# Kernel tuning notes

Hardware: AMD Instinct MI355X
Metric: run time of the kernel (lower is better)

## Reference

```python
import jax, jax.numpy as jnp
import numpy as np

D_MODEL = 2048
N_HEADS = 16
D_K = D_MODEL // N_HEADS
MAX_SEQ_LEN = 2048


def _rotary_tables(dim, max_seq_len):
    angular_freq = (1.0 / 10000.0) ** jnp.linspace(0.0, 1.0, dim // 2, dtype=jnp.float32)
    t = jnp.arange(max_seq_len, dtype=jnp.float32)
    theta = jnp.einsum('i,j->ij', t, angular_freq)  # [S, dk/2]
    return jnp.cos(theta), jnp.sin(theta)


def _apply_rotary(x, cos, sin):
    # x: [B, H, S, dk]; cos/sin: [S, dk/2]
    seq_len = x.shape[-2]
    c = cos[:seq_len][None, None]
    s = sin[:seq_len][None, None]
    x1, x2 = jnp.split(x, 2, axis=-1)
    y1 = x1 * c - x2 * s
    y2 = x1 * s + x2 * c
    return jnp.concatenate([y1, y2], axis=-1).astype(x.dtype)


def setup_inputs() -> dict:
    key = jax.random.key(0)
    k_x, k_qkv, k_o = jax.random.split(key, 3)
    B, S = 2, 2048
    x = jax.random.normal(k_x, (B, S, D_MODEL), dtype=jnp.float32)
    scale = 1.0 / np.sqrt(D_MODEL)
    w_qkv = jax.random.normal(k_qkv, (3 * D_MODEL, D_MODEL), dtype=jnp.float32) * scale
    w_o = jax.random.normal(k_o, (D_MODEL, D_MODEL), dtype=jnp.float32) * scale
    return {"x": x, "w_qkv": w_qkv, "w_o": w_o}


def reference(x, w_qkv, w_o):
    B, S, _ = x.shape
    cos, sin = _rotary_tables(D_K, MAX_SEQ_LEN)
    qkv = jnp.einsum('bsd,ed->bse', x, w_qkv)  # [B, S, 3*d_model]
    qkv = qkv.reshape(B, S, 3, N_HEADS, D_K).transpose(2, 0, 3, 1, 4)  # [3,B,H,S,dk]
    Q, K, V = qkv[0], qkv[1], qkv[2]
    Q = _apply_rotary(Q, cos, sin)
    K = _apply_rotary(K, cos, sin)
    scale = 1.0 / np.sqrt(D_K)
    scores = jnp.einsum('bhqd,bhkd->bhqk', Q, K) * scale
    causal = jnp.tril(jnp.ones((S, S), dtype=bool))
    scores = jnp.where(causal[None, None], scores, jnp.finfo(scores.dtype).min)
    attn = jax.nn.softmax(scores, axis=-1)
    out = jnp.einsum('bhqk,bhkd->bhqd', attn, V)  # [B,H,S,dk]
    out = out.transpose(0, 2, 1, 3).reshape(B, S, D_MODEL)
    return jnp.einsum('bsd,ed->bse', out, w_o)
```

## Files before the change

### kernel.cpp

```cpp
#include <hip/hip_runtime.h>
#include <hip/hip_bf16.h>


typedef __bf16 bf16;
typedef __bf16 bf16x4 __attribute__((ext_vector_type(4)));
typedef __bf16 bf16x8 __attribute__((ext_vector_type(8)));
typedef float f32x4 __attribute__((ext_vector_type(4)));
typedef float f32x16 __attribute__((ext_vector_type(16)));
typedef int i32x4 __attribute__((ext_vector_type(4)));

#define DEV __device__ __forceinline__

DEV void gll16(const void* g, void* lds_base_wave_uniform) {
  __builtin_amdgcn_global_load_lds((const __attribute__((address_space(1))) void*)g,
                                   (__attribute__((address_space(3))) void*)lds_base_wave_uniform,
                                   16, 0, 0);
}

DEV f32x4 mfma16(bf16x8 a, bf16x8 b, f32x4 c) {
  return __builtin_amdgcn_mfma_f32_16x16x32_bf16(a, b, c, 0, 0, 0);
}
DEV f32x16 mfma32(bf16x8 a, bf16x8 b, f32x16 c) {
  return __builtin_amdgcn_mfma_f32_32x32x16_bf16(a, b, c, 0, 0, 0);
}

DEV int cvtpk(float lo, float hi) {
  int r;
  asm("v_cvt_pk_bf16_f32 %0, %1, %2" : "=v"(r) : "v"(lo), "v"(hi));
  return r;
}

__global__ __launch_bounds__(256) void prep_all(const float* __restrict__ x,
                                                const float* __restrict__ wqkv,
                                                const float* __restrict__ wo,
                                                bf16* __restrict__ xb,
                                                bf16* __restrict__ wqkvb,
                                                bf16* __restrict__ wob,
                                                float* __restrict__ ctab,
                                                float* __restrict__ stab) {
  const int b = blockIdx.x;
  if (b < 12288) {
    const float* in;
    bf16* out;
    int bb = b;
    if (b < 4096) {
      in = x; out = xb;
    } else if (b < 10240) {
      in = wqkv; out = wqkvb; bb -= 4096;
    } else {
      in = wo; out = wob; bb -= 10240;
    }
    const int i = (bb * 256 + threadIdx.x) << 3;
    float4 a = *(const float4*)(in + i);
    float4 c = *(const float4*)(in + i + 4);
    bf16x8 o;
    o[0] = (bf16)a.x; o[1] = (bf16)a.y; o[2] = (bf16)a.z; o[3] = (bf16)a.w;
    o[4] = (bf16)c.x; o[5] = (bf16)c.y; o[6] = (bf16)c.z; o[7] = (bf16)c.w;
    *(bf16x8*)(out + i) = o;
  } else {
    const int id = (b - 12288) * 256 + threadIdx.x;
    const int s = id >> 6, j = id & 63;
    float freq = powf(10000.0f, -(float)j / 63.0f);
    float th = (float)s * freq;
    ctab[id] = cosf(th);
    stab[id] = sinf(th);
  }
}

__global__ __launch_bounds__(512, 2) void gemm384(const bf16* __restrict__ A,
                                                  const bf16* __restrict__ Bt,
                                                  bf16* __restrict__ q_out,
                                                  bf16* __restrict__ k_out,
                                                  bf16* __restrict__ v_out,
                                                  const float* __restrict__ ctab,
                                                  const float* __restrict__ stab) {
  constexpr int K = 2048, NKT = 64;
  constexpr int BUFB = 40960;
  __shared__ char lds[3 * BUFB];
  const int id = blockIdx.x;
  const int swz = (id & 7) * 32 + (id >> 3);
  const int bx = swz & 15, by = swz >> 4;
  const int m0 = by << 8;
  const int n0 = bx * 384;
  const int tid = threadIdx.x, w = tid >> 6, l = tid & 63;
  const int wm = w >> 2, wn = w & 3;
  const int lsl = (l & 7) ^ ((l >> 3) & 7);
  const int srow = ((l >> 3) << 1) + (lsl >> 2);
  const int scol = (lsl & 3) << 3;

  auto STAGE = [&](int t, char* base) {
    const int k0 = t << 5;
#pragma unroll
    for (int c = 0; c < 2; ++c) {
      const int row = (c << 7) + (w << 4) + srow;
      gll16(A + (size_t)(m0 + row) * K + k0 + scol, base + (c << 13) + (w << 10));
    }
#pragma unroll
    for (int c = 0; c < 3; ++c) {
      const int row = (c << 7) + (w << 4) + srow;
      gll16(Bt + (size_t)(n0 + row) * K + k0 + scol, base + 16384 + (c << 13) + (w << 10));
    }
  };

  f32x4 acc[8][6] = {};

  STAGE(0, (char*)lds);
  STAGE(1, (char*)lds + BUFB);
  asm volatile("s_waitcnt vmcnt(5)" ::: "memory");
  __builtin_amdgcn_s_barrier();

#pragma unroll 1
  for (int t = 0, bi = 0, bj = 2; t < NKT; ++t) {
    char* rbase = (char*)lds + bi * BUFB;
    bf16x8 bfr[6];
#pragma unroll
    for (int j = 0; j < 6; ++j) {
      const int row = ((j >> 1) << 7) + ((j & 1) << 6) + (wn << 4) + (l & 15);
      const int sr = row >> 1;
      bfr[j] = *(const bf16x8*)(rbase + 16384 + sr * 128 +
                                (((((row & 1) << 2) | (l >> 4)) ^ (sr & 7)) << 4));
    }
    bf16x8 af[4];
#pragma unroll
    for (int i = 0; i < 4; ++i) {
      const int row = (wm << 7) + (i << 4) + (l & 15);
      const int sr = row >> 1;
      af[i] = *(const bf16x8*)(rbase + sr * 128 +
                               (((((row & 1) << 2) | (l >> 4)) ^ (sr & 7)) << 4));
    }
    if (t + 2 < NKT) STAGE(t + 2, (char*)lds + bj * BUFB);
    asm volatile("s_waitcnt lgkmcnt(0)" ::: "memory");
    __builtin_amdgcn_sched_barrier(0);
    __builtin_amdgcn_s_setprio(1);
#pragma unroll
    for (int i = 0; i < 4; ++i)
#pragma unroll
      for (int j = 0; j < 6; ++j)
        acc[i][j] = mfma16(af[i], bfr[j], acc[i][j]);
    __builtin_amdgcn_s_setprio(0);
#pragma unroll
    for (int i = 0; i < 4; ++i) {
      const int row = (wm << 7) + 64 + (i << 4) + (l & 15);
      const int sr = row >> 1;
      af[i] = *(const bf16x8*)(rbase + sr * 128 +
                               (((((row & 1) << 2) | (l >> 4)) ^ (sr & 7)) << 4));
    }
    asm volatile("s_waitcnt lgkmcnt(0)" ::: "memory");
    __builtin_amdgcn_sched_barrier(0);
    __builtin_amdgcn_s_setprio(1);
#pragma unroll
    for (int i = 0; i < 4; ++i)
#pragma unroll
      for (int j = 0; j < 6; ++j)
        acc[4 + i][j] = mfma16(af[i], bfr[j], acc[4 + i][j]);
    __builtin_amdgcn_s_setprio(0);
    if (t + 2 < NKT) {
      asm volatile("s_waitcnt vmcnt(5)" ::: "memory");
    } else if (t + 2 == NKT) {
      asm volatile("s_waitcnt vmcnt(0)" ::: "memory");
    }
    __builtin_amdgcn_sched_barrier(0);
    __builtin_amdgcn_s_barrier();
    bi = (bi == 2) ? 0 : bi + 1;
    bj = (bj == 2) ? 0 : bj + 1;
  }

  const int d2 = (wn << 4) + (l & 15);
#pragma unroll
  for (int i = 0; i < 8; ++i) {
    const int mbase = m0 + (wm << 7) + (i << 4) + ((l >> 4) << 2);
    const int b_ = mbase >> 11, sbase = mbase & 2047;
    float cc[4], ss[4];
    if (((n0 + 256) >> 11) == 1 || (n0 >> 11) == 1) {
#pragma unroll
      for (int r = 0; r < 4; ++r) {
        cc[r] = ctab[((sbase + r) << 6) + d2];
        ss[r] = stab[((sbase + r) << 6) + d2];
      }
    }
#pragma unroll
    for (int p = 0; p < 3; ++p) {
      const int nb = n0 + (p << 7);
      const int which = nb >> 11;
      const int h = (nb >> 7) & 15;
      if (which == 0) {
        const size_t base = (((size_t)((b_ << 4) | h)) * 2048 + sbase) * 128;
#pragma unroll
        for (int r = 0; r < 4; ++r) {
          q_out[base + ((size_t)r << 7) + d2]      = (bf16)acc[i][2 * p][r];
          q_out[base + ((size_t)r << 7) + d2 + 64] = (bf16)acc[i][2 * p + 1][r];
        }
      } else if (which == 1) {
        const size_t base = (((size_t)((b_ << 4) | h)) * 2048 + sbase) * 128;
#pragma unroll
        for (int r = 0; r < 4; ++r) {
          const float x1 = acc[i][2 * p][r], x2 = acc[i][2 * p + 1][r];
          k_out[base + ((size_t)r << 7) + d2]      = (bf16)(x1 * cc[r] - x2 * ss[r]);
          k_out[base + ((size_t)r << 7) + d2 + 64] = (bf16)(x1 * ss[r] + x2 * cc[r]);
        }
      } else {
        bf16x4 v1, v2;
#pragma unroll
        for (int r = 0; r < 4; ++r) {
          v1[r] = (bf16)acc[i][2 * p][r];
          v2[r] = (bf16)acc[i][2 * p + 1][r];
        }
        const size_t hb = ((size_t)((b_ << 4) | h) << 18);
        *(bf16x4*)(v_out + hb + ((size_t)d2 << 11) + sbase) = v1;
        *(bf16x4*)(v_out + hb + ((size_t)(d2 + 64) << 11) + sbase) = v2;
      }
    }
  }
}

template <int NTN>
__global__ __launch_bounds__(256, 2) void gemm_o(const bf16* __restrict__ A,
                                                 const bf16* __restrict__ Bt,
                                                 float* __restrict__ f_out) {
  constexpr int K = 2048, NKT = 64;
  constexpr int BUFB = 16384;
  __shared__ char lds[3 * BUFB];
  const int nwg = 32 * NTN;
  const int id = blockIdx.x;
  const int swz = (id & 7) * (nwg >> 3) + (id >> 3);
  const int bx = swz % NTN, by = swz / NTN;
  const int m0 = by << 7, n0 = bx << 7;
  const int tid = threadIdx.x, w = tid >> 6, l = tid & 63;
  const int wm = w >> 1, wn = w & 1;
  const int lsl = (l & 7) ^ ((l >> 3) & 7);
  const int srow = ((l >> 3) << 1) + (lsl >> 2);
  const int scol = (lsl & 3) << 3;

  auto STAGE = [&](int t, char* base) {
    const int k0 = t << 5;
#pragma unroll
    for (int c = 0; c < 2; ++c) {
      const int row = (c << 6) + (w << 4) + srow;
      gll16(A + (size_t)(m0 + row) * K + k0 + scol, base + (c << 12) + (w << 10));
      gll16(Bt + (size_t)(n0 + row) * K + k0 + scol, base + 8192 + (c << 12) + (w << 10));
    }
  };

  f32x4 acc[4][4] = {};

  STAGE(0, (char*)lds);
  STAGE(1, (char*)lds + BUFB);
  asm volatile("s_waitcnt vmcnt(4)" ::: "memory");
  __builtin_amdgcn_s_barrier();

#pragma unroll 1
  for (int t = 0, bi = 0, bj = 2; t < NKT; ++t) {
    char* rbase = (char*)lds + bi * BUFB;
    bf16x8 af[4], bfr[4];
#pragma unroll
    for (int i = 0; i < 4; ++i) {
      const int row = (wm << 6) + (i << 4) + (l & 15);
      const int sr = row >> 1;
      af[i] = *(const bf16x8*)(rbase + sr * 128 +
                               (((((row & 1) << 2) | (l >> 4)) ^ (sr & 7)) << 4));
    }
#pragma unroll
    for (int j = 0; j < 4; ++j) {
      const int row = (wn << 6) + (j << 4) + (l & 15);
      const int sr = row >> 1;
      bfr[j] = *(const bf16x8*)(rbase + 8192 + sr * 128 +
                                (((((row & 1) << 2) | (l >> 4)) ^ (sr & 7)) << 4));
    }
    if (t + 2 < NKT) STAGE(t + 2, (char*)lds + bj * BUFB);
    asm volatile("s_waitcnt lgkmcnt(0)" ::: "memory");
    __builtin_amdgcn_sched_barrier(0);
    __builtin_amdgcn_s_setprio(1);
#pragma unroll
    for (int i = 0; i < 4; ++i)
#pragma unroll
      for (int j = 0; j < 4; ++j)
        acc[i][j] = mfma16(af[i], bfr[j], acc[i][j]);
    __builtin_amdgcn_s_setprio(0);
    if (t + 2 < NKT) {
      asm volatile("s_waitcnt vmcnt(4)" ::: "memory");
    } else if (t + 2 == NKT) {
      asm volatile("s_waitcnt vmcnt(0)" ::: "memory");
    }
    __builtin_amdgcn_sched_barrier(0);
    __builtin_amdgcn_s_barrier();
    bi = (bi == 2) ? 0 : bi + 1;
    bj = (bj == 2) ? 0 : bj + 1;
  }

#pragma unroll
  for (int i = 0; i < 4; ++i)
#pragma unroll
    for (int j = 0; j < 4; ++j)
#pragma unroll
      for (int r = 0; r < 4; ++r) {
        const int m = m0 + (wm << 6) + (i << 4) + ((l >> 4) << 2) + r;
        const int n = n0 + (wn << 6) + (j << 4) + (l & 15);
        f_out[(size_t)m * 2048 + n] = acc[i][j][r];
      }
}

__global__ __launch_bounds__(256) void attn_kernel(const bf16* __restrict__ Qb,
                                                   const bf16* __restrict__ Kb,
                                                   const bf16* __restrict__ Vt,
                                                   bf16* __restrict__ Ao,
                                                   const float* __restrict__ ctab,
                                                   const float* __restrict__ stab) {
  constexpr int S = 2048;
  __shared__ bf16 Ks[2][128 * 128];
  __shared__ bf16 Vs[2][128 * 128];
  const int id = blockIdx.x;
  const int swz = (id & 7) * 32 + (id >> 3);
  const int bh = swz >> 3;
  const int pp = swz & 7;
  const int ntA = pp + 1;
  const int NT = 17;
  const int tid = threadIdx.x, w = tid >> 6, l = tid & 63;
  const int hi = l >> 5;
  const bf16* Qp = Qb + ((size_t)bh << 18);
  const bf16* Kp = Kb + ((size_t)bh << 18);
  const bf16* Vp = Vt + ((size_t)bh << 18);

  auto KVSEQ = [&](int ti) { return ((ti < ntA) ? ti : ti - ntA) << 7; };

  auto STAGE_KV = [&](int kv0, int bufi) {
    char* Kbase = (char*)Ks + (bufi << 15);
    char* Vbase = (char*)Vs + (bufi << 15);
#pragma unroll
    for (int i = 0; i < 8; ++i) {
      const int rk = (w << 5) + (i << 2) + (l >> 4);
      gll16(Kp + ((size_t)(kv0 + rk) << 7) + (((l & 15) ^ (rk & 7)) << 3),
            Kbase + (w << 13) + (i << 10));
      const int rv = rk;
      gll16(Vp + (size_t)rv * S + kv0 + (((l & 15) ^ (rv & 7)) << 3),
            Vbase + (w << 13) + (i << 10));
    }
  };

  bf16x8 qf[8];
  auto LOAD_Q = [&](int q0_) {
    const int sq = q0_ + (w << 5) + (l & 31);
#pragma unroll
    for (int kt = 0; kt < 8; ++kt)
      qf[kt] = *(const bf16x8*)(Qp + ((size_t)sq << 7) + (kt << 4) + (hi << 3));
    const float QS = 0.08838834764831845f * 1.4426950408889634f;
#pragma unroll
    for (int kt = 0; kt < 4; ++kt) {
      const int d2 = (kt << 4) + (hi << 3);
      const float* cp = ctab + (sq << 6) + d2;
      const float* sp = stab + (sq << 6) + d2;
      float4 c0 = *(const float4*)cp, c1 = *(const float4*)(cp + 4);
      float4 s0 = *(const float4*)sp, s1 = *(const float4*)(sp + 4);
      const float cA[8] = {c0.x, c0.y, c0.z, c0.w, c1.x, c1.y, c1.z, c1.w};
      const float sA[8] = {s0.x, s0.y, s0.z, s0.w, s1.x, s1.y, s1.z, s1.w};
      const bf16x8 lo = qf[kt], up = qf[kt + 4];
#pragma unroll
      for (int j2 = 0; j2 < 8; ++j2) {
        const float a = (float)lo[j2], b2 = (float)up[j2];
        qf[kt][j2]     = (bf16)((a * cA[j2] - b2 * sA[j2]) * QS);
        qf[kt + 4][j2] = (bf16)((a * sA[j2] + b2 * cA[j2]) * QS);
      }
    }
  };

  f32x16 o[4] = {};
  float mrun = -3e38f, lrun = 0.f;
  int q0 = pp << 7;

  auto EPILOGUE = [&](int q0_) {
    const float rinv = 1.0f / lrun;
    const int b = bh >> 4, h = bh & 15;
    const int sq = q0_ + (w << 5) + (l & 31);
    bf16* Arow = Ao + (((size_t)(b * S + sq)) << 11) + (h << 7);
#pragma unroll
    for (int dt = 0; dt < 4; ++dt)
#pragma unroll
      for (int g = 0; g < 4; ++g) {
        bf16x4 ov;
#pragma unroll
        for (int r = 0; r < 4; ++r) ov[r] = (bf16)(o[dt][(g << 2) + r] * rinv);
        *(bf16x4*)(Arow + (dt << 5) + (g << 3) + (hi << 2)) = ov;
      }
  };

  STAGE_KV(KVSEQ(0), 0);
  LOAD_Q(q0);
  __syncthreads();

  int bufi = 0;
#pragma unroll 1
  for (int ti = 0; ti < NT; ++ti, bufi ^= 1) {
    if (ti + 1 < NT) STAGE_KV(KVSEQ(ti + 1), bufi ^ 1);
    const int kv0 = KVSEQ(ti);
    const int qminw = q0 + (w << 5);
    {
      const char* Kbase = (const char*)Ks + (bufi << 15);
      const char* Vbase = (const char*)Vs + (bufi << 15);
      f32x16 sc[4] = {};
      __builtin_amdgcn_s_setprio(1);
#pragma unroll
      for (int kt = 0; kt < 8; ++kt) {
        const int rk0 = l & 31;
        const int coff = (kt << 5) + (hi << 4);
        const int cswz = coff ^ ((rk0 & 7) << 4);
#pragma unroll
        for (int nt = 0; nt < 4; ++nt) {
          bf16x8 kf = *(const bf16x8*)(Kbase + ((rk0 + (nt << 5)) << 8) + cswz);
          sc[nt] = mfma32(kf, qf[kt], sc[nt]);
        }
      }
      __builtin_amdgcn_s_setprio(0);
      if (kv0 + 127 > qminw) {
        const int qg = qminw + (l & 31);
#pragma unroll
        for (int nt = 0; nt < 4; ++nt)
#pragma unroll
          for (int r = 0; r < 16; ++r) {
            const int kvr = kv0 + (nt << 5) + (r & 3) + ((r >> 2) << 3) + (hi << 2);
            if (kvr > qg) sc[nt][r] = -3e38f;
          }
      }
      f32x16 mm;
#pragma unroll
      for (int r = 0; r < 16; ++r)
        mm[r] = fmaxf(fmaxf(sc[0][r], sc[1][r]), fmaxf(sc[2][r], sc[3][r]));
#pragma unroll
      for (int off = 8; off; off >>= 1)
#pragma unroll
        for (int r = 0; r < off; ++r) mm[r] = fmaxf(mm[r], mm[r + off]);
      float mx = mm[0];
      mx = fmaxf(mx, __shfl_xor(mx, 32));
      const float mnew = fmaxf(mrun, mx);
      if (!__all(mx <= mrun)) {
        const float alpha = exp2f(mrun - mnew);
        lrun *= alpha;
#pragma unroll
        for (int dt = 0; dt < 4; ++dt) o[dt] *= alpha;
      }
      mrun = mnew;
      float p0 = 0.f, p1 = 0.f, p2 = 0.f, p3 = 0.f;
#pragma unroll
      for (int nt = 0; nt < 4; ++nt)
#pragma unroll
        for (int r = 0; r < 16; r += 4) {
          sc[nt][r]     = exp2f(sc[nt][r] - mnew);     p0 += sc[nt][r];
          sc[nt][r + 1] = exp2f(sc[nt][r + 1] - mnew); p1 += sc[nt][r + 1];
          sc[nt][r + 2] = exp2f(sc[nt][r + 2] - mnew); p2 += sc[nt][r + 2];
          sc[nt][r + 3] = exp2f(sc[nt][r + 3] - mnew); p3 += sc[nt][r + 3];
        }
      float ps = (p0 + p1) + (p2 + p3);
      ps += __shfl_xor(ps, 32);
      lrun += ps;
#pragma unroll
      for (int ks = 0; ks < 8; ++ks) {
        const f32x16& s = sc[ks >> 1];
        const int rbp = (ks & 1) << 3;
        int pa_ = cvtpk(s[rbp + 0], s[rbp + 1]);
        int pb_ = cvtpk(s[rbp + 2], s[rbp + 3]);
        int pc_ = cvtpk(s[rbp + 4], s[rbp + 5]);
        int pd_ = cvtpk(s[rbp + 6], s[rbp + 7]);
        int sa = __shfl_xor(pa_, 32), sb2 = __shfl_xor(pb_, 32);
        int sc_ = __shfl_xor(pc_, 32), sd = __shfl_xor(pd_, 32);
        i32x4 pi;
        pi[0] = hi ? sc_ : pa_;
        pi[1] = hi ? sd : pb_;
        pi[2] = hi ? pc_ : sa;
        pi[3] = hi ? pd_ : sb2;
        const bf16x8 pf = __builtin_bit_cast(bf16x8, pi);
        __builtin_amdgcn_s_setprio(1);
#pragma unroll
        for (int dt = 0; dt < 4; ++dt) {
          const int rd = (dt << 5) + (l & 31);
          const bf16x8 vf = *(const bf16x8*)(Vbase + (rd << 8) +
                                             (((ks << 5) + (hi << 4)) ^ ((rd & 7) << 4)));
          o[dt] = mfma32(vf, pf, o[dt]);
        }
        __builtin_amdgcn_s_setprio(0);
      }
    }
    if (ti == ntA - 1) {
      EPILOGUE(q0);
      q0 = (15 - pp) << 7;
#pragma unroll
      for (int dt = 0; dt < 4; ++dt)
#pragma unroll
        for (int r = 0; r < 16; ++r) o[dt][r] = 0.f;
      mrun = -3e38f; lrun = 0.f;
      LOAD_Q(q0);
    }
    __syncthreads();
  }
  EPILOGUE(q0);
}

extern "C" void kernel_launch(void* const* d_in, const int* in_sizes, int n_in,
                              void* d_out, int out_size, void* d_ws, size_t ws_size,
                              hipStream_t stream) {
  const float* x = (const float*)d_in[0];
  const float* w_qkv = (const float*)d_in[1];
  const float* w_o = (const float*)d_in[2];
  float* out = (float*)d_out;
  char* ws = (char*)d_ws;

  bf16* xb    = (bf16*)(ws);
  bf16* wqkvb = (bf16*)(ws + (16ull << 20));
  bf16* wob   = (bf16*)(ws + (40ull << 20));
  bf16* Qb    = (bf16*)(ws + (48ull << 20));
  bf16* Kb    = (bf16*)(ws + (64ull << 20));
  bf16* Vt    = (bf16*)(ws + (80ull << 20));
  bf16* Ao    = (bf16*)(ws + (96ull << 20));
  float* ctab = (float*)(ws + (112ull << 20));
  float* stab = (float*)(ws + (113ull << 20));

  prep_all<<<12800, 256, 0, stream>>>(x, w_qkv, w_o, xb, wqkvb, wob, ctab, stab);
  gemm384<<<256, 512, 0, stream>>>(xb, wqkvb, Qb, Kb, Vt, ctab, stab);
  attn_kernel<<<256, 256, 0, stream>>>(Qb, Kb, Vt, Ao, ctab, stab);
  gemm_o<16><<<512, 256, 0, stream>>>(Ao, wob, out);
}
```

Baseline: 244.4 us.

## Split attention KV tile across two wave groups and merge partial softmax results

Attention blocks grow from 4 to 8 waves. Each group of four waves handles half of every 128-row KV tile for the same query rows, and the two partial (m, l, O) states are merged through LDS at the epilogue. The aim is more waves per CU to hide latency and skip fully masked half-tiles on the diagonal. The cost is extra synchronization, an LDS round trip with bf16 rounding of one partial output, and higher register pressure from the 512-thread, two-block launch bounds.

```diff
diff --git a/kernel.cpp b/kernel.cpp
--- a/kernel.cpp
+++ b/kernel.cpp
@@ -299,15 +299,14 @@
       }
 }
 
-__global__ __launch_bounds__(256) void attn_kernel(const bf16* __restrict__ Qb,
-                                                   const bf16* __restrict__ Kb,
-                                                   const bf16* __restrict__ Vt,
-                                                   bf16* __restrict__ Ao,
-                                                   const float* __restrict__ ctab,
-                                                   const float* __restrict__ stab) {
+__global__ __launch_bounds__(512, 2) void attn_kernel(const bf16* __restrict__ Qb,
+                                                      const bf16* __restrict__ Kb,
+                                                      const bf16* __restrict__ Vt,
+                                                      bf16* __restrict__ Ao,
+                                                      const float* __restrict__ ctab,
+                                                      const float* __restrict__ stab) {
   constexpr int S = 2048;
-  __shared__ bf16 Ks[2][128 * 128];
-  __shared__ bf16 Vs[2][128 * 128];
+  __shared__ char lds[2][65536];
   const int id = blockIdx.x;
   const int swz = (id & 7) * 32 + (id >> 3);
   const int bh = swz >> 3;
@@ -315,6 +314,7 @@
   const int ntA = pp + 1;
   const int NT = 17;
   const int tid = threadIdx.x, w = tid >> 6, l = tid & 63;
+  const int wq = w & 3, half = w >> 2;
   const int hi = l >> 5;
   const bf16* Qp = Qb + ((size_t)bh << 18);
   const bf16* Kp = Kb + ((size_t)bh << 18);
@@ -323,22 +323,34 @@
   auto KVSEQ = [&](int ti) { return ((ti < ntA) ? ti : ti - ntA) << 7; };
 
   auto STAGE_KV = [&](int kv0, int bufi) {
-    char* Kbase = (char*)Ks + (bufi << 15);
-    char* Vbase = (char*)Vs + (bufi << 15);
-#pragma unroll
-    for (int i = 0; i < 8; ++i) {
-      const int rk = (w << 5) + (i << 2) + (l >> 4);
-      gll16(Kp + ((size_t)(kv0 + rk) << 7) + (((l & 15) ^ (rk & 7)) << 3),
-            Kbase + (w << 13) + (i << 10));
-      const int rv = rk;
-      gll16(Vp + (size_t)rv * S + kv0 + (((l & 15) ^ (rv & 7)) << 3),
-            Vbase + (w << 13) + (i << 10));
+    char* Kbase = lds[bufi];
+    char* Vbase = lds[bufi] + 32768;
+#pragma unroll
+    for (int i = 0; i < 2; ++i) {
+      const int rk = (w << 4) + (i << 3) + ((l >> 4) << 1) + (i == 0 ? 0 : 0);
+      (void)rk;
+    }
+#pragma unroll
+    for (int i = 0; i < 2; ++i) {
+    }
+#pragma unroll
+    for (int i = 0; i < 2; ++i) {
+      const int r0 = (w << 4) + (i << 3) + (l >> 4);
+      const int r1 = r0 + 4;
+      gll16(Kp + ((size_t)(kv0 + r0) << 7) + (((l & 15) ^ (r0 & 7)) << 3),
+            Kbase + (w << 12) + (i << 11));
+      gll16(Kp + ((size_t)(kv0 + r1) << 7) + (((l & 15) ^ (r1 & 7)) << 3),
+            Kbase + (w << 12) + (i << 11) + 1024);
+      gll16(Vp + (size_t)r0 * S + kv0 + (((l & 15) ^ (r0 & 7)) << 3),
+            Vbase + (w << 12) + (i << 11));
+      gll16(Vp + (size_t)r1 * S + kv0 + (((l & 15) ^ (r1 & 7)) << 3),
+            Vbase + (w << 12) + (i << 11) + 1024);
     }
   };
 
   bf16x8 qf[8];
   auto LOAD_Q = [&](int q0_) {
-    const int sq = q0_ + (w << 5) + (l & 31);
+    const int sq = q0_ + (wq << 5) + (l & 31);
 #pragma unroll
     for (int kt = 0; kt < 8; ++kt)
       qf[kt] = *(const bf16x8*)(Qp + ((size_t)sq << 7) + (kt << 4) + (hi << 3));
@@ -366,20 +378,53 @@
   float mrun = -3e38f, lrun = 0.f;
   int q0 = pp << 7;
 
-  auto EPILOGUE = [&](int q0_) {
-    const float rinv = 1.0f / lrun;
-    const int b = bh >> 4, h = bh & 15;
-    const int sq = q0_ + (w << 5) + (l & 31);
-    bf16* Arow = Ao + (((size_t)(b * S + sq)) << 11) + (h << 7);
-#pragma unroll
-    for (int dt = 0; dt < 4; ++dt)
-#pragma unroll
-      for (int g = 0; g < 4; ++g) {
-        bf16x4 ov;
-#pragma unroll
-        for (int r = 0; r < 4; ++r) ov[r] = (bf16)(o[dt][(g << 2) + r] * rinv);
-        *(bf16x4*)(Arow + (dt << 5) + (g << 3) + (hi << 2)) = ov;
-      }
+  auto MERGE_EPI = [&](int q0_, char* scratch) {
+    bf16* ob = (bf16*)scratch;
+    float* ml = (float*)(scratch + 36864);
+    __syncthreads();
+    if (half == 1) {
+      bf16* dst = ob + ((wq << 6) + l) * 72;
+#pragma unroll
+      for (int dt = 0; dt < 4; ++dt) {
+        bf16x8 t0, t1;
+#pragma unroll
+        for (int e = 0; e < 8; ++e) { t0[e] = (bf16)o[dt][e]; t1[e] = (bf16)o[dt][8 + e]; }
+        *(bf16x8*)(dst + (dt << 4)) = t0;
+        *(bf16x8*)(dst + (dt << 4) + 8) = t1;
+      }
+      if (l < 32) {
+        ml[(wq << 5) + l] = mrun;
+        ml[128 + (wq << 5) + l] = lrun;
+      }
+    }
+    __syncthreads();
+    if (half == 0) {
+      const float mhi = ml[(wq << 5) + (l & 31)];
+      const float lhi = ml[128 + (wq << 5) + (l & 31)];
+      const float ms = fmaxf(mrun, mhi);
+      const float alo = exp2f(mrun - ms), ahi = exp2f(mhi - ms);
+      const float rinv = 1.0f / (lrun * alo + lhi * ahi);
+      const bf16* src = ob + ((wq << 6) + l) * 72;
+      const int b = bh >> 4, h = bh & 15;
+      const int sq = q0_ + (wq << 5) + (l & 31);
+      bf16* Arow = Ao + (((size_t)(b * S + sq)) << 11) + (h << 7);
+#pragma unroll
+      for (int dt = 0; dt < 4; ++dt) {
+        bf16x8 h0 = *(const bf16x8*)(src + (dt << 4));
+        bf16x8 h1 = *(const bf16x8*)(src + (dt << 4) + 8);
+#pragma unroll
+        for (int g = 0; g < 4; ++g) {
+          bf16x4 ov;
+#pragma unroll
+          for (int r = 0; r < 4; ++r) {
+            const int e = (g << 2) + r;
+            const float hv = (e < 8) ? (float)h0[e] : (float)h1[e - 8];
+            ov[r] = (bf16)((o[dt][e] * alo + hv * ahi) * rinv);
+          }
+          *(bf16x4*)(Arow + (dt << 5) + (g << 3) + (hi << 2)) = ov;
+        }
+      }
+    }
   };
 
   STAGE_KV(KVSEQ(0), 0);
@@ -391,38 +436,35 @@
   for (int ti = 0; ti < NT; ++ti, bufi ^= 1) {
     if (ti + 1 < NT) STAGE_KV(KVSEQ(ti + 1), bufi ^ 1);
     const int kv0 = KVSEQ(ti);
-    const int qminw = q0 + (w << 5);
-    {
-      const char* Kbase = (const char*)Ks + (bufi << 15);
-      const char* Vbase = (const char*)Vs + (bufi << 15);
-      f32x16 sc[4] = {};
+    const int kvh0 = kv0 + (half << 6);
+    const int qminw = q0 + (wq << 5);
+    if (kvh0 <= qminw + 31) {
+      const char* Kbase = lds[bufi];
+      const char* Vbase = lds[bufi] + 32768;
+      f32x16 sc0 = {}, sc1 = {};
       __builtin_amdgcn_s_setprio(1);
 #pragma unroll
       for (int kt = 0; kt < 8; ++kt) {
-        const int rk0 = l & 31;
+        const int rk0 = (l & 31) + (half << 6);
         const int coff = (kt << 5) + (hi << 4);
-        const int cswz = coff ^ ((rk0 & 7) << 4);
-#pragma unroll
-        for (int nt = 0; nt < 4; ++nt) {
-          bf16x8 kf = *(const bf16x8*)(Kbase + ((rk0 + (nt << 5)) << 8) + cswz);
-          sc[nt] = mfma32(kf, qf[kt], sc[nt]);
+        bf16x8 k0 = *(const bf16x8*)(Kbase + (rk0 << 8) + (coff ^ ((rk0 & 7) << 4)));
+        bf16x8 k1 = *(const bf16x8*)(Kbase + ((rk0 + 32) << 8) + (coff ^ (((rk0 + 32) & 7) << 4)));
+        sc0 = mfma32(k0, qf[kt], sc0);
+        sc1 = mfma32(k1, qf[kt], sc1);
+      }
+      __builtin_amdgcn_s_setprio(0);
+      if (kvh0 + 63 > qminw) {
+        const int qg = qminw + (l & 31);
+#pragma unroll
+        for (int r = 0; r < 16; ++r) {
+          const int kvr = kvh0 + (r & 3) + ((r >> 2) << 3) + (hi << 2);
+          if (kvr > qg) sc0[r] = -3e38f;
+          if (kvr + 32 > qg) sc1[r] = -3e38f;
         }
       }
-      __builtin_amdgcn_s_setprio(0);
-      if (kv0 + 127 > qminw) {
-        const int qg = qminw + (l & 31);
-#pragma unroll
-        for (int nt = 0; nt < 4; ++nt)
-#pragma unroll
-          for (int r = 0; r < 16; ++r) {
-            const int kvr = kv0 + (nt << 5) + (r & 3) + ((r >> 2) << 3) + (hi << 2);
-            if (kvr > qg) sc[nt][r] = -3e38f;
-          }
-      }
       f32x16 mm;
 #pragma unroll
-      for (int r = 0; r < 16; ++r)
-        mm[r] = fmaxf(fmaxf(sc[0][r], sc[1][r]), fmaxf(sc[2][r], sc[3][r]));
+      for (int r = 0; r < 16; ++r) mm[r] = fmaxf(sc0[r], sc1[r]);
 #pragma unroll
       for (int off = 8; off; off >>= 1)
 #pragma unroll
@@ -439,20 +481,17 @@
       mrun = mnew;
       float p0 = 0.f, p1 = 0.f, p2 = 0.f, p3 = 0.f;
 #pragma unroll
-      for (int nt = 0; nt < 4; ++nt)
-#pragma unroll
-        for (int r = 0; r < 16; r += 4) {
-          sc[nt][r]     = exp2f(sc[nt][r] - mnew);     p0 += sc[nt][r];
-          sc[nt][r + 1] = exp2f(sc[nt][r + 1] - mnew); p1 += sc[nt][r + 1];
-          sc[nt][r + 2] = exp2f(sc[nt][r + 2] - mnew); p2 += sc[nt][r + 2];
-          sc[nt][r + 3] = exp2f(sc[nt][r + 3] - mnew); p3 += sc[nt][r + 3];
-        }
+      for (int r = 0; r < 16; r += 2) {
+        sc0[r] = exp2f(sc0[r] - mnew); sc0[r + 1] = exp2f(sc0[r + 1] - mnew);
+        sc1[r] = exp2f(sc1[r] - mnew); sc1[r + 1] = exp2f(sc1[r + 1] - mnew);
+        p0 += sc0[r]; p1 += sc0[r + 1]; p2 += sc1[r]; p3 += sc1[r + 1];
+      }
       float ps = (p0 + p1) + (p2 + p3);
       ps += __shfl_xor(ps, 32);
       lrun += ps;
 #pragma unroll
-      for (int ks = 0; ks < 8; ++ks) {
-        const f32x16& s = sc[ks >> 1];
+      for (int ks = 0; ks < 4; ++ks) {
+        const f32x16& s = (ks & 2) ? sc1 : sc0;
         const int rbp = (ks & 1) << 3;
         int pa_ = cvtpk(s[rbp + 0], s[rbp + 1]);
         int pb_ = cvtpk(s[rbp + 2], s[rbp + 3]);
@@ -470,15 +509,16 @@
 #pragma unroll
         for (int dt = 0; dt < 4; ++dt) {
           const int rd = (dt << 5) + (l & 31);
+          const int coffv = (half << 7) + (ks << 5) + (hi << 4);
           const bf16x8 vf = *(const bf16x8*)(Vbase + (rd << 8) +
-                                             (((ks << 5) + (hi << 4)) ^ ((rd & 7) << 4)));
+                                             (coffv ^ ((rd & 7) << 4)));
           o[dt] = mfma32(vf, pf, o[dt]);
         }
         __builtin_amdgcn_s_setprio(0);
       }
     }
     if (ti == ntA - 1) {
-      EPILOGUE(q0);
+      MERGE_EPI(q0, lds[bufi]);
       q0 = (15 - pp) << 7;
 #pragma unroll
       for (int dt = 0; dt < 4; ++dt)
@@ -489,7 +529,7 @@
     }
     __syncthreads();
   }
-  EPILOGUE(q0);
+  MERGE_EPI(q0, lds[(NT - 1) & 1]);
 }
 
 extern "C" void kernel_launch(void* const* d_in, const int* in_sizes, int n_in,
@@ -513,6 +553,6 @@
 
   prep_all<<<12800, 256, 0, stream>>>(x, w_qkv, w_o, xb, wqkvb, wob, ctab, stab);
   gemm384<<<256, 512, 0, stream>>>(xb, wqkvb, Qb, Kb, Vt, ctab, stab);
-  attn_kernel<<<256, 256, 0, stream>>>(Qb, Kb, Vt, Ao, ctab, stab);
+  attn_kernel<<<256, 512, 0, stream>>>(Qb, Kb, Vt, Ao, ctab, stab);
   gemm_o<16><<<512, 256, 0, stream>>>(Ao, wob, out);
 }
```

Result: faster. 227.4 us (-7.0%).
